# Performance work log

Measured on AMD Instinct MI355X. Metric: run time of the kernel, lower is better.

## Reference

```python
import jax, jax.numpy as jnp
import numpy as np

N = 50000      # nodes
E = 800000     # edges (before self-loops)
IN = 256       # input features
H = 8          # heads
C = 32         # hidden channels per head
OUT = 40       # classes
NEG_SLOPE = 0.2


def setup_inputs() -> dict:
    key = jax.random.key(0)
    ks = jax.random.split(key, 12)
    sd = lambda k, sh: (jax.random.normal(k, sh, jnp.float32) * 0.05)
    return {
        "x": jax.random.normal(ks[0], (N, IN), jnp.float32),
        "edge_index": jax.random.randint(ks[1], (2, E), 0, N),
        "W1": sd(ks[2], (IN, H * C)),
        "a_src1": sd(ks[3], (H, C)),
        "a_dst1": sd(ks[4], (H, C)),
        "b1": jnp.zeros((C,), jnp.float32),
        "W2": sd(ks[5], (C, H * C)),
        "a_src2": sd(ks[6], (H, C)),
        "a_dst2": sd(ks[7], (H, C)),
        "b2": jnp.zeros((C,), jnp.float32),
        "Wo": sd(ks[8], (C, OUT)),
        "bo": jnp.zeros((OUT,), jnp.float32),
    }


def gat_layer(x, src, dst, n, W, a_src, a_dst, b):
    # x: [N, F]; src/dst: [E'] (self-loops included). concat=False -> mean over heads.
    h = (x @ W).reshape(n, H, C)                       # [N, H, C]
    alpha_src = jnp.sum(h * a_src, axis=-1)            # [N, H]
    alpha_dst = jnp.sum(h * a_dst, axis=-1)            # [N, H]
    e = alpha_src[src] + alpha_dst[dst]                # [E', H]
    e = jnp.where(e > 0, e, NEG_SLOPE * e)             # leaky_relu
    # segment softmax over incoming edges of each dst node
    m = jax.ops.segment_max(e, dst, num_segments=n)    # [N, H]
    ex = jnp.exp(e - m[dst])                           # [E', H]
    s = jax.ops.segment_sum(ex, dst, num_segments=n)   # [N, H]
    alpha = ex / s[dst]                                # [E', H]
    msg = alpha[:, :, None] * h[src]                   # [E', H, C]
    out = jax.ops.segment_sum(msg, dst, num_segments=n)  # [N, H, C]
    return out.mean(axis=1) + b                        # [N, C]


def reference(x, edge_index, W1, a_src1, a_dst1, b1, W2, a_src2, a_dst2, b2, Wo, bo):
    n = x.shape[0]
    loops = jnp.arange(n, dtype=edge_index.dtype)
    src = jnp.concatenate([edge_index[0], loops])      # add self-loops (PyG default)
    dst = jnp.concatenate([edge_index[1], loops])
    h = gat_layer(x, src, dst, n, W1, a_src1, a_dst1, b1)
    h = jax.nn.elu(h)                                  # dropout skipped (eval)
    h = gat_layer(h, src, dst, n, W2, a_src2, a_dst2, b2)
    h = jax.nn.elu(h)
    logits = h @ Wo + bo
    return jax.nn.log_softmax(logits, axis=1)
```

## Files before the change

### kernel.cpp

```cpp
#include <hip/hip_runtime.h>
#include <math.h>

#define N_NODES 50000
#define N_PAD   50016
#define N_EDGES 800000
#define E_TOT   (N_EDGES + N_NODES)
#define F_IN    256
#define NHEAD   8
#define CH      32
#define HC      256
#define OUT_C   40
#define NEG_SLOPE 0.2f
#define CAP     64
#define G_WCVT  ((HC * F_IN + 255) / 256)
#define G_WCVT2 ((HC * CH + 255) / 256)
#define NRANGE  8
#define RANGE_SZ (N_NODES / NRANGE)
#define BIN_CHUNK 2048
#define G_BINCH ((E_TOT + BIN_CHUNK - 1) / BIN_CHUNK)
#define G_BIN   (G_BINCH * NRANGE)

typedef unsigned short u16;
typedef unsigned int   u32;
typedef unsigned char  u8;
typedef __attribute__((ext_vector_type(8))) short bf16x8;
typedef __attribute__((ext_vector_type(4))) float f32x4;
typedef __attribute__((ext_vector_type(2))) float f32x2;

__device__ __forceinline__ u16 f2bf(float f) {
    union { u32 u; float f; } x; x.f = f;
    u32 u = x.u;
    return (u16)((u + 0x7fffu + ((u >> 16) & 1u)) >> 16);
}
__device__ __forceinline__ float bflo(u32 v) {
    union { u32 u; float f; } x; x.u = v << 16; return x.f;
}
__device__ __forceinline__ u8 f2fp8(float f) {
    return (u8)(__builtin_amdgcn_cvt_pk_fp8_f32(f, f, 0, false) & 0xff);
}


__global__ __launch_bounds__(256) void prep_kernel(const int* __restrict__ ei,
        int* __restrict__ cursor, u16* __restrict__ csr_src,
        const float* __restrict__ W1, u16* __restrict__ Wt,
        const float* __restrict__ W2, u16* __restrict__ W2t) {
    int b = blockIdx.x;
    if (b < G_BIN) {
        const int r  = b & (NRANGE - 1);
        const int ch = b >> 3;
        const int lo = r * RANGE_SZ, hi = lo + RANGE_SZ;
        int j0 = ch * BIN_CHUNK + threadIdx.x;
        #pragma unroll
        for (int i = 0; i < BIN_CHUNK / 256; ++i) {
            int j = j0 + i * 256;
            if (j < E_TOT) {
                int d = (j < N_EDGES) ? ei[N_EDGES + j] : (j - N_EDGES);
                if (d >= lo && d < hi) {
                    int s = (j < N_EDGES) ? ei[j] : d;
                    int pos = atomicAdd(&cursor[d], 1);
                    if (pos < CAP) csr_src[d * CAP + pos] = (u16)s;
                }
            }
        }
    } else if (b < G_BIN + G_WCVT) {
        int t = (b - G_BIN) * 256 + threadIdx.x;
        int n = t & 255, k = t >> 8;
        Wt[(size_t)n * F_IN + k] = f2bf(W1[(size_t)k * HC + n]);
    } else {
        int t = (b - G_BIN - G_WCVT) * 256 + threadIdx.x;
        if (t >= HC * CH) return;
        int n = t & 255, k = t >> 8;
        W2t[(size_t)n * CH + k] = f2bf(W2[(size_t)k * HC + n]);
    }
}

__device__ __forceinline__ void gemm_epilogue(f32x4 acc[2][4], int row0, int quad,
        int l16, int nb, const float* __restrict__ a_src,
        const float* __restrict__ a_dst, u8* __restrict__ ht8,
        float* __restrict__ asrc, float* __restrict__ adst) {
    #pragma unroll
    for (int m = 0; m < 2; ++m) {
        #pragma unroll
        for (int r = 0; r < 4; ++r) {
            int row = row0 + m * 16 + quad * 4 + r;
            if (row < N_NODES) {
                u8* hr = ht8 + (size_t)row * HC;
                #pragma unroll
                for (int n = 0; n < 4; ++n)
                    hr[nb + n * 16 + l16] = f2fp8(acc[m][n][r]);
            }
        }
    }
    const int hA = nb >> 5;
    const float sA0 = a_src[hA * 32 + l16],       sA1 = a_src[hA * 32 + 16 + l16];
    const float sB0 = a_src[(hA + 1) * 32 + l16], sB1 = a_src[(hA + 1) * 32 + 16 + l16];
    const float dA0 = a_dst[hA * 32 + l16],       dA1 = a_dst[hA * 32 + 16 + l16];
    const float dB0 = a_dst[(hA + 1) * 32 + l16], dB1 = a_dst[(hA + 1) * 32 + 16 + l16];
    #pragma unroll
    for (int m = 0; m < 2; ++m) {
        #pragma unroll
        for (int r = 0; r < 4; ++r) {
            float pa = acc[m][0][r] * sA0 + acc[m][1][r] * sA1;
            float pb = acc[m][2][r] * sB0 + acc[m][3][r] * sB1;
            float qa = acc[m][0][r] * dA0 + acc[m][1][r] * dA1;
            float qb = acc[m][2][r] * dB0 + acc[m][3][r] * dB1;
            #pragma unroll
            for (int off = 1; off < 16; off <<= 1) {
                pa += __shfl_xor(pa, off, 64);
                pb += __shfl_xor(pb, off, 64);
                qa += __shfl_xor(qa, off, 64);
                qb += __shfl_xor(qb, off, 64);
            }
            int row = row0 + m * 16 + quad * 4 + r;
            if (l16 == 0 && row < N_NODES) {
                asrc[row * NHEAD + hA]     = pa;
                asrc[row * NHEAD + hA + 1] = pb;
                adst[row * NHEAD + hA]     = qa;
                adst[row * NHEAD + hA + 1] = qb;
            }
        }
    }
}

__global__ __launch_bounds__(256) void gemm1_mfma(const float* __restrict__ x,
        const u16* __restrict__ Wt, const float* __restrict__ a_src,
        const float* __restrict__ a_dst, u8* __restrict__ ht8,
        float* __restrict__ asrc, float* __restrict__ adst) {
    __shared__ u16 As[32 * 256];
    const int row0 = blockIdx.x * 32;
    const int t    = threadIdx.x;

    {
        const int r   = t >> 3;
        const int sub = t & 7;
        const int gr  = min(row0 + r, N_NODES - 1);
        const float4* xr = (const float4*)(x + (size_t)gr * F_IN);
        const int sw = (r & 7) << 4;
        char* Ar = (char*)As + r * 512;
        #pragma unroll
        for (int i = 0; i < 8; ++i) {
            int f4 = i * 8 + sub;
            float4 v = xr[f4];
            u32 lo = (u32)f2bf(v.x) | ((u32)f2bf(v.y) << 16);
            u32 hi = (u32)f2bf(v.z) | ((u32)f2bf(v.w) << 16);
            *(uint2*)(Ar + ((f4 * 8) ^ sw)) = make_uint2(lo, hi);
        }
    }
    __syncthreads();

    const int wave = t >> 6;
    const int lane = t & 63;
    const int l16  = lane & 15;
    const int quad = lane >> 4;
    const int nb   = wave * 64;
    const int swr  = (l16 & 7) << 4;
    const char* Ab = (const char*)As;

    f32x4 acc[2][4];
    #pragma unroll
    for (int m = 0; m < 2; ++m)
        #pragma unroll
        for (int n = 0; n < 4; ++n) acc[m][n] = (f32x4){0.f, 0.f, 0.f, 0.f};

    const u16* bp = Wt + (size_t)(nb + l16) * F_IN;

    #pragma unroll 1
    for (int k0 = 0; k0 < F_IN; k0 += 32) {
        const int ko = k0 + quad * 8;
        bf16x8 a0 = *(const bf16x8*)(Ab + l16 * 512 + ((ko * 2) ^ swr));
        bf16x8 a1 = *(const bf16x8*)(Ab + (16 + l16) * 512 + ((ko * 2) ^ swr));
        bf16x8 b0 = *(const bf16x8*)(bp + 0 * 16 * F_IN + ko);
        bf16x8 b1 = *(const bf16x8*)(bp + 1 * 16 * F_IN + ko);
        bf16x8 b2 = *(const bf16x8*)(bp + 2 * 16 * F_IN + ko);
        bf16x8 b3 = *(const bf16x8*)(bp + 3 * 16 * F_IN + ko);
        acc[0][0] = __builtin_amdgcn_mfma_f32_16x16x32_bf16(a0, b0, acc[0][0], 0, 0, 0);
        acc[0][1] = __builtin_amdgcn_mfma_f32_16x16x32_bf16(a0, b1, acc[0][1], 0, 0, 0);
        acc[0][2] = __builtin_amdgcn_mfma_f32_16x16x32_bf16(a0, b2, acc[0][2], 0, 0, 0);
        acc[0][3] = __builtin_amdgcn_mfma_f32_16x16x32_bf16(a0, b3, acc[0][3], 0, 0, 0);
        acc[1][0] = __builtin_amdgcn_mfma_f32_16x16x32_bf16(a1, b0, acc[1][0], 0, 0, 0);
        acc[1][1] = __builtin_amdgcn_mfma_f32_16x16x32_bf16(a1, b1, acc[1][1], 0, 0, 0);
        acc[1][2] = __builtin_amdgcn_mfma_f32_16x16x32_bf16(a1, b2, acc[1][2], 0, 0, 0);
        acc[1][3] = __builtin_amdgcn_mfma_f32_16x16x32_bf16(a1, b3, acc[1][3], 0, 0, 0);
    }
    gemm_epilogue(acc, row0, quad, l16, nb, a_src, a_dst, ht8, asrc, adst);
}

__global__ __launch_bounds__(256) void gemm2_mfma(const u16* __restrict__ hmb,
        const u16* __restrict__ W2t, const float* __restrict__ a_src,
        const float* __restrict__ a_dst, u8* __restrict__ ht8,
        float* __restrict__ asrc, float* __restrict__ adst) {
    const int row0 = blockIdx.x * 32;
    const int t    = threadIdx.x;
    const int wave = t >> 6;
    const int lane = t & 63;
    const int l16  = lane & 15;
    const int quad = lane >> 4;
    const int nb   = wave * 64;
    const int ko   = quad * 8;

    const u16* a0p = hmb + (size_t)(row0 + l16) * CH;
    const u16* a1p = a0p + 16 * CH;
    const u16* bp  = W2t + (size_t)(nb + l16) * CH;

    bf16x8 a0 = *(const bf16x8*)(a0p + ko);
    bf16x8 a1 = *(const bf16x8*)(a1p + ko);
    bf16x8 b0 = *(const bf16x8*)(bp + 0 * 16 * CH + ko);
    bf16x8 b1 = *(const bf16x8*)(bp + 1 * 16 * CH + ko);
    bf16x8 b2 = *(const bf16x8*)(bp + 2 * 16 * CH + ko);
    bf16x8 b3 = *(const bf16x8*)(bp + 3 * 16 * CH + ko);

    f32x4 z = (f32x4){0.f, 0.f, 0.f, 0.f};
    f32x4 acc[2][4];
    acc[0][0] = __builtin_amdgcn_mfma_f32_16x16x32_bf16(a0, b0, z, 0, 0, 0);
    acc[0][1] = __builtin_amdgcn_mfma_f32_16x16x32_bf16(a0, b1, z, 0, 0, 0);
    acc[0][2] = __builtin_amdgcn_mfma_f32_16x16x32_bf16(a0, b2, z, 0, 0, 0);
    acc[0][3] = __builtin_amdgcn_mfma_f32_16x16x32_bf16(a0, b3, z, 0, 0, 0);
    acc[1][0] = __builtin_amdgcn_mfma_f32_16x16x32_bf16(a1, b0, z, 0, 0, 0);
    acc[1][1] = __builtin_amdgcn_mfma_f32_16x16x32_bf16(a1, b1, z, 0, 0, 0);
    acc[1][2] = __builtin_amdgcn_mfma_f32_16x16x32_bf16(a1, b2, z, 0, 0, 0);
    acc[1][3] = __builtin_amdgcn_mfma_f32_16x16x32_bf16(a1, b3, z, 0, 0, 0);

    gemm_epilogue(acc, row0, quad, l16, nb, a_src, a_dst, ht8, asrc, adst);
}

__global__ __launch_bounds__(256) void attn_kernel(const int* __restrict__ degp,
        const u16* __restrict__ csr_src, const float* __restrict__ asrc,
        const float* __restrict__ adst, const u8* __restrict__ ht8,
        const float* __restrict__ b, u16* __restrict__ out) {
    const int wid = (blockIdx.x * 256 + threadIdx.x) >> 6;
    if (wid >= N_NODES) return;
    const int dst  = wid;
    const int lane = threadIdx.x & 63;
    const int q    = lane >> 4;
    const int l16  = lane & 15;
    const int h    = l16 >> 1;
    const float ad_own = adst[dst * NHEAD + h];
    const u8* hbase = ht8 + l16 * 16;

    f32x2 acc2[8];
    #pragma unroll
    for (int i = 0; i < 8; ++i) acc2[i] = (f32x2){0.f, 0.f};
    float wsum = 0.f;

    const int cnt = min(degp[dst], CAP);
    const int p0 = dst * CAP, p1 = p0 + cnt;
    const int nt = (cnt + 7) >> 3;

    float asA = -1e30f, asB = -1e30f;
    uint4 hvA = make_uint4(0u, 0u, 0u, 0u), hvB = make_uint4(0u, 0u, 0u, 0u);
    int e = p0 + q;
    if (e < p1) {
        int s = (int)csr_src[e];
        asA = asrc[s * NHEAD + h];
        hvA = *(const uint4*)(hbase + ((size_t)s << 8));
    }
    if (e + 4 < p1) {
        int s = (int)csr_src[e + 4];
        asB = asrc[s * NHEAD + h];
        hvB = *(const uint4*)(hbase + ((size_t)s << 8));
    }

    for (int it = 0; it < nt; ++it) {
        float aA = asA; uint4 hA = hvA;
        float aB = asB; uint4 hB = hvB;
        asA = -1e30f; asB = -1e30f;
        if (e + 8 < p1) {
            int s = (int)csr_src[e + 8];
            asA = asrc[s * NHEAD + h];
            hvA = *(const uint4*)(hbase + ((size_t)s << 8));
        }
        if (e + 12 < p1) {
            int s = (int)csr_src[e + 12];
            asB = asrc[s * NHEAD + h];
            hvB = *(const uint4*)(hbase + ((size_t)s << 8));
        }
        {
            float x = aA + ad_own;
            x = x > 0.f ? x : NEG_SLOPE * x;
            float w = __expf(x);
            wsum += w;
            f32x2 w2; w2.x = w; w2.y = w;
            acc2[0] = __builtin_elementwise_fma(w2, __builtin_amdgcn_cvt_pk_f32_fp8(hA.x, false), acc2[0]);
            acc2[1] = __builtin_elementwise_fma(w2, __builtin_amdgcn_cvt_pk_f32_fp8(hA.x, true ), acc2[1]);
            acc2[2] = __builtin_elementwise_fma(w2, __builtin_amdgcn_cvt_pk_f32_fp8(hA.y, false), acc2[2]);
            acc2[3] = __builtin_elementwise_fma(w2, __builtin_amdgcn_cvt_pk_f32_fp8(hA.y, true ), acc2[3]);
            acc2[4] = __builtin_elementwise_fma(w2, __builtin_amdgcn_cvt_pk_f32_fp8(hA.z, false), acc2[4]);
            acc2[5] = __builtin_elementwise_fma(w2, __builtin_amdgcn_cvt_pk_f32_fp8(hA.z, true ), acc2[5]);
            acc2[6] = __builtin_elementwise_fma(w2, __builtin_amdgcn_cvt_pk_f32_fp8(hA.w, false), acc2[6]);
            acc2[7] = __builtin_elementwise_fma(w2, __builtin_amdgcn_cvt_pk_f32_fp8(hA.w, true ), acc2[7]);
        }
        {
            float x = aB + ad_own;
            x = x > 0.f ? x : NEG_SLOPE * x;
            float w = __expf(x);
            wsum += w;
            f32x2 w2; w2.x = w; w2.y = w;
            acc2[0] = __builtin_elementwise_fma(w2, __builtin_amdgcn_cvt_pk_f32_fp8(hB.x, false), acc2[0]);
            acc2[1] = __builtin_elementwise_fma(w2, __builtin_amdgcn_cvt_pk_f32_fp8(hB.x, true ), acc2[1]);
            acc2[2] = __builtin_elementwise_fma(w2, __builtin_amdgcn_cvt_pk_f32_fp8(hB.y, false), acc2[2]);
            acc2[3] = __builtin_elementwise_fma(w2, __builtin_amdgcn_cvt_pk_f32_fp8(hB.y, true ), acc2[3]);
            acc2[4] = __builtin_elementwise_fma(w2, __builtin_amdgcn_cvt_pk_f32_fp8(hB.z, false), acc2[4]);
            acc2[5] = __builtin_elementwise_fma(w2, __builtin_amdgcn_cvt_pk_f32_fp8(hB.z, true ), acc2[5]);
            acc2[6] = __builtin_elementwise_fma(w2, __builtin_amdgcn_cvt_pk_f32_fp8(hB.w, false), acc2[6]);
            acc2[7] = __builtin_elementwise_fma(w2, __builtin_amdgcn_cvt_pk_f32_fp8(hB.w, true ), acc2[7]);
        }
        e += 8;
    }

    #pragma unroll
    for (int i = 0; i < 8; ++i) {
        acc2[i].x += __shfl_xor(acc2[i].x, 16, 64);
        acc2[i].y += __shfl_xor(acc2[i].y, 16, 64);
        acc2[i].x += __shfl_xor(acc2[i].x, 32, 64);
        acc2[i].y += __shfl_xor(acc2[i].y, 32, 64);
    }
    wsum += __shfl_xor(wsum, 16, 64);
    wsum += __shfl_xor(wsum, 32, 64);

    float winv = 1.0f / wsum;
    f32x2 winv2; winv2.x = winv; winv2.y = winv;
    #pragma unroll
    for (int i = 0; i < 8; ++i) acc2[i] *= winv2;

    #pragma unroll
    for (int i = 0; i < 8; ++i) {
        acc2[i].x += __shfl_xor(acc2[i].x, 2, 64);
        acc2[i].y += __shfl_xor(acc2[i].y, 2, 64);
        acc2[i].x += __shfl_xor(acc2[i].x, 4, 64);
        acc2[i].y += __shfl_xor(acc2[i].y, 4, 64);
        acc2[i].x += __shfl_xor(acc2[i].x, 8, 64);
        acc2[i].y += __shfl_xor(acc2[i].y, 8, 64);
    }

    if (lane < 2) {
        const int c0 = lane * 16;
        const float4* bp4 = (const float4*)(b + c0);
        float4 b0 = bp4[0], b1 = bp4[1], b2 = bp4[2], b3 = bp4[3];
        float bb[16] = {b0.x, b0.y, b0.z, b0.w, b1.x, b1.y, b1.z, b1.w,
                        b2.x, b2.y, b2.z, b2.w, b3.x, b3.y, b3.z, b3.w};
        u32 d[8];
        #pragma unroll
        for (int i = 0; i < 8; ++i) {
            float v0 = acc2[i].x * 0.125f + bb[2 * i];
            float v1 = acc2[i].y * 0.125f + bb[2 * i + 1];
            v0 = v0 > 0.f ? v0 : (__expf(v0) - 1.f);
            v1 = v1 > 0.f ? v1 : (__expf(v1) - 1.f);
            d[i] = (u32)f2bf(v0) | ((u32)f2bf(v1) << 16);
        }
        uint4* op = (uint4*)(out + (size_t)dst * CH + c0);
        op[0] = make_uint4(d[0], d[1], d[2], d[3]);
        op[1] = make_uint4(d[4], d[5], d[6], d[7]);
    }
}

__global__ __launch_bounds__(256) void out_kernel(const u16* __restrict__ hf,
        const float* __restrict__ Wo, const float* __restrict__ bo,
        float* __restrict__ out) {
    const int wave = threadIdx.x >> 6;
    const int lane = threadIdx.x & 63;
    const int n    = blockIdx.x * 4 + wave;
    __shared__ float hs[4][CH];
    if (n < N_NODES && lane < CH) hs[wave][lane] = bflo((u32)hf[n * CH + lane]);
    __syncthreads();
    if (n >= N_NODES) return;
    float logit = -INFINITY;
    if (lane < OUT_C) {
        float a = bo[lane];
        #pragma unroll
        for (int k = 0; k < CH; ++k) a += hs[wave][k] * Wo[k * OUT_C + lane];
        logit = a;
    }
    float m = logit;
    #pragma unroll
    for (int off = 32; off; off >>= 1) m = fmaxf(m, __shfl_xor(m, off, 64));
    float ex = (lane < OUT_C) ? __expf(logit - m) : 0.f;
    float ssum = ex;
    #pragma unroll
    for (int off = 32; off; off >>= 1) ssum += __shfl_xor(ssum, off, 64);
    if (lane < OUT_C) out[(size_t)n * OUT_C + lane] = logit - m - __logf(ssum);
}

extern "C" void kernel_launch(void* const* d_in, const int* in_sizes, int n_in,
                              void* d_out, int out_size, void* d_ws, size_t ws_size,
                              hipStream_t stream) {
    const float* x      = (const float*)d_in[0];
    const int*   ei     = (const int*)  d_in[1];
    const float* W1     = (const float*)d_in[2];
    const float* a_src1 = (const float*)d_in[3];
    const float* a_dst1 = (const float*)d_in[4];
    const float* b1     = (const float*)d_in[5];
    const float* W2     = (const float*)d_in[6];
    const float* a_src2 = (const float*)d_in[7];
    const float* a_dst2 = (const float*)d_in[8];
    const float* b2     = (const float*)d_in[9];
    const float* Wo     = (const float*)d_in[10];
    const float* bo     = (const float*)d_in[11];
    float* out = (float*)d_out;

    char* ws = (char*)d_ws;
    size_t off = 0;
    auto carve = [&](size_t bytes) { char* p = ws + off; off += (bytes + 255) & ~(size_t)255; return p; };
    u8*    ht8     = (u8*)   carve((size_t)N_NODES * HC);
    u16*   Wt      = (u16*)  carve((size_t)HC * F_IN * 2);
    u16*   W2t     = (u16*)  carve((size_t)HC * CH * 2);
    float* asrc    = (float*)carve((size_t)N_NODES * NHEAD * 4);
    float* adst    = (float*)carve((size_t)N_NODES * NHEAD * 4);
    u16*   hmid    = (u16*)  carve((size_t)N_PAD * CH * 2);
    u16*   hout    = (u16*)  carve((size_t)N_NODES * CH * 2);
    int*   cursor  = (int*)  carve((size_t)N_NODES * 4);
    u16*   csr_src = (u16*)  carve((size_t)N_NODES * CAP * 2);

    const int g_prep  = G_BIN + G_WCVT + G_WCVT2;
    const int g_gemm  = (N_NODES + 31) / 32;
    const int g_attn  = (N_NODES * 64 + 255) / 256;
    const int g_out   = (N_NODES + 3) / 4;

    (void)hipMemsetAsync(cursor, 0, (size_t)N_NODES * 4, stream);
    prep_kernel<<<g_prep, 256, 0, stream>>>(ei, cursor, csr_src, W1, Wt, W2, W2t);

    gemm1_mfma<<<g_gemm, 256, 0, stream>>>(x, Wt, a_src1, a_dst1, ht8, asrc, adst);
    attn_kernel<<<g_attn, 256, 0, stream>>>(cursor, csr_src, asrc, adst, ht8, b1, hmid);

    gemm2_mfma<<<g_gemm, 256, 0, stream>>>(hmid, W2t, a_src2, a_dst2, ht8, asrc, adst);
    attn_kernel<<<g_attn, 256, 0, stream>>>(cursor, csr_src, asrc, adst, ht8, b2, hout);

    out_kernel<<<g_out, 256, 0, stream>>>(hout, Wo, bo, out);
}
```

Baseline: 317.2 us.

## Sort per-node neighbor lists and fuse final attention with output head

Adds a bitonic sort kernel that orders each destination's source indices, so gathers from ht8 follow a more sequential, cache-friendly pattern and the CSR order becomes deterministic. It also fuses the second attention aggregation with the bias/ELU, output linear layer and log-softmax into one kernel, which removes the hout round trip and one launch. The fused kernel skips max subtraction in the softmax, which assumes the scores stay small enough not to overflow. The extra sort pass costs one read and write of the CSR array.

```diff
diff --git a/kernel.cpp b/kernel.cpp
--- a/kernel.cpp
+++ b/kernel.cpp
@@ -72,6 +72,26 @@
         int n = t & 255, k = t >> 8;
         W2t[(size_t)n * CH + k] = f2bf(W2[(size_t)k * HC + n]);
     }
+}
+
+__global__ __launch_bounds__(256) void sort_kernel(const int* __restrict__ cursor,
+        u16* __restrict__ csr_src) {
+    const int dst  = (blockIdx.x * 256 + threadIdx.x) >> 6;
+    if (dst >= N_NODES) return;
+    const int lane = threadIdx.x & 63;
+    const int cnt  = min(cursor[dst], CAP);
+    u32 v = (lane < cnt) ? (u32)csr_src[dst * CAP + lane] : 0x7FFFFFFFu;
+    #pragma unroll
+    for (int k = 2; k <= 64; k <<= 1) {
+        #pragma unroll
+        for (int j = k >> 1; j > 0; j >>= 1) {
+            u32 pv = (u32)__shfl_xor((int)v, j, 64);
+            bool asc      = ((lane & k) == 0);
+            bool keep_min = (((lane & j) == 0) == asc);
+            v = keep_min ? min(v, pv) : max(v, pv);
+        }
+    }
+    if (lane < cnt) csr_src[dst * CAP + lane] = (u16)v;
 }
 
 __device__ __forceinline__ void gemm_epilogue(f32x4 acc[2][4], int row0, int quad,
@@ -353,31 +373,145 @@
     }
 }
 
-__global__ __launch_bounds__(256) void out_kernel(const u16* __restrict__ hf,
-        const float* __restrict__ Wo, const float* __restrict__ bo,
-        float* __restrict__ out) {
-    const int wave = threadIdx.x >> 6;
+__global__ __launch_bounds__(256) void attn_fin_kernel(const int* __restrict__ degp,
+        const u16* __restrict__ csr_src, const float* __restrict__ asrc,
+        const float* __restrict__ adst, const u8* __restrict__ ht8,
+        const float* __restrict__ b, const float* __restrict__ Wo,
+        const float* __restrict__ bo, float* __restrict__ out) {
+    const int dst  = (blockIdx.x * 256 + threadIdx.x) >> 6;
     const int lane = threadIdx.x & 63;
-    const int n    = blockIdx.x * 4 + wave;
-    __shared__ float hs[4][CH];
-    if (n < N_NODES && lane < CH) hs[wave][lane] = bflo((u32)hf[n * CH + lane]);
+    const int w4   = threadIdx.x >> 6;
+    const int q    = lane >> 4;
+    const int l16  = lane & 15;
+    const int h    = l16 >> 1;
+    const float ad_own = adst[dst * NHEAD + h];
+    const u8* hbase = ht8 + l16 * 16;
+
+    __shared__ float hsm[4][CH];
+
+    f32x2 acc2[8];
+    #pragma unroll
+    for (int i = 0; i < 8; ++i) acc2[i] = (f32x2){0.f, 0.f};
+    float wsum = 0.f;
+
+    const int cnt = min(degp[dst], CAP);
+    const int p0 = dst * CAP, p1 = p0 + cnt;
+    const int nt = (cnt + 7) >> 3;
+
+    float asA = -1e30f, asB = -1e30f;
+    uint4 hvA = make_uint4(0u, 0u, 0u, 0u), hvB = make_uint4(0u, 0u, 0u, 0u);
+    int e = p0 + q;
+    if (e < p1) {
+        int s = (int)csr_src[e];
+        asA = asrc[s * NHEAD + h];
+        hvA = *(const uint4*)(hbase + ((size_t)s << 8));
+    }
+    if (e + 4 < p1) {
+        int s = (int)csr_src[e + 4];
+        asB = asrc[s * NHEAD + h];
+        hvB = *(const uint4*)(hbase + ((size_t)s << 8));
+    }
+
+    for (int it = 0; it < nt; ++it) {
+        float aA = asA; uint4 hA = hvA;
+        float aB = asB; uint4 hB = hvB;
+        asA = -1e30f; asB = -1e30f;
+        if (e + 8 < p1) {
+            int s = (int)csr_src[e + 8];
+            asA = asrc[s * NHEAD + h];
+            hvA = *(const uint4*)(hbase + ((size_t)s << 8));
+        }
+        if (e + 12 < p1) {
+            int s = (int)csr_src[e + 12];
+            asB = asrc[s * NHEAD + h];
+            hvB = *(const uint4*)(hbase + ((size_t)s << 8));
+        }
+        {
+            float x = aA + ad_own;
+            x = x > 0.f ? x : NEG_SLOPE * x;
+            float w = __expf(x);
+            wsum += w;
+            f32x2 w2; w2.x = w; w2.y = w;
+            acc2[0] = __builtin_elementwise_fma(w2, __builtin_amdgcn_cvt_pk_f32_fp8(hA.x, false), acc2[0]);
+            acc2[1] = __builtin_elementwise_fma(w2, __builtin_amdgcn_cvt_pk_f32_fp8(hA.x, true ), acc2[1]);
+            acc2[2] = __builtin_elementwise_fma(w2, __builtin_amdgcn_cvt_pk_f32_fp8(hA.y, false), acc2[2]);
+            acc2[3] = __builtin_elementwise_fma(w2, __builtin_amdgcn_cvt_pk_f32_fp8(hA.y, true ), acc2[3]);
+            acc2[4] = __builtin_elementwise_fma(w2, __builtin_amdgcn_cvt_pk_f32_fp8(hA.z, false), acc2[4]);
+            acc2[5] = __builtin_elementwise_fma(w2, __builtin_amdgcn_cvt_pk_f32_fp8(hA.z, true ), acc2[5]);
+            acc2[6] = __builtin_elementwise_fma(w2, __builtin_amdgcn_cvt_pk_f32_fp8(hA.w, false), acc2[6]);
+            acc2[7] = __builtin_elementwise_fma(w2, __builtin_amdgcn_cvt_pk_f32_fp8(hA.w, true ), acc2[7]);
+        }
+        {
+            float x = aB + ad_own;
+            x = x > 0.f ? x : NEG_SLOPE * x;
+            float w = __expf(x);
+            wsum += w;
+            f32x2 w2; w2.x = w; w2.y = w;
+            acc2[0] = __builtin_elementwise_fma(w2, __builtin_amdgcn_cvt_pk_f32_fp8(hB.x, false), acc2[0]);
+            acc2[1] = __builtin_elementwise_fma(w2, __builtin_amdgcn_cvt_pk_f32_fp8(hB.x, true ), acc2[1]);
+            acc2[2] = __builtin_elementwise_fma(w2, __builtin_amdgcn_cvt_pk_f32_fp8(hB.y, false), acc2[2]);
+            acc2[3] = __builtin_elementwise_fma(w2, __builtin_amdgcn_cvt_pk_f32_fp8(hB.y, true ), acc2[3]);
+            acc2[4] = __builtin_elementwise_fma(w2, __builtin_amdgcn_cvt_pk_f32_fp8(hB.z, false), acc2[4]);
+            acc2[5] = __builtin_elementwise_fma(w2, __builtin_amdgcn_cvt_pk_f32_fp8(hB.z, true ), acc2[5]);
+            acc2[6] = __builtin_elementwise_fma(w2, __builtin_amdgcn_cvt_pk_f32_fp8(hB.w, false), acc2[6]);
+            acc2[7] = __builtin_elementwise_fma(w2, __builtin_amdgcn_cvt_pk_f32_fp8(hB.w, true ), acc2[7]);
+        }
+        e += 8;
+    }
+
+    #pragma unroll
+    for (int i = 0; i < 8; ++i) {
+        acc2[i].x += __shfl_xor(acc2[i].x, 16, 64);
+        acc2[i].y += __shfl_xor(acc2[i].y, 16, 64);
+        acc2[i].x += __shfl_xor(acc2[i].x, 32, 64);
+        acc2[i].y += __shfl_xor(acc2[i].y, 32, 64);
+    }
+    wsum += __shfl_xor(wsum, 16, 64);
+    wsum += __shfl_xor(wsum, 32, 64);
+
+    float winv = 1.0f / wsum;
+    f32x2 winv2; winv2.x = winv; winv2.y = winv;
+    #pragma unroll
+    for (int i = 0; i < 8; ++i) acc2[i] *= winv2;
+
+    #pragma unroll
+    for (int i = 0; i < 8; ++i) {
+        acc2[i].x += __shfl_xor(acc2[i].x, 2, 64);
+        acc2[i].y += __shfl_xor(acc2[i].y, 2, 64);
+        acc2[i].x += __shfl_xor(acc2[i].x, 4, 64);
+        acc2[i].y += __shfl_xor(acc2[i].y, 4, 64);
+        acc2[i].x += __shfl_xor(acc2[i].x, 8, 64);
+        acc2[i].y += __shfl_xor(acc2[i].y, 8, 64);
+    }
+
+    if (lane < 2) {
+        #pragma unroll
+        for (int i = 0; i < 8; ++i) {
+            hsm[w4][lane * 16 + 2 * i]     = acc2[i].x * 0.125f;
+            hsm[w4][lane * 16 + 2 * i + 1] = acc2[i].y * 0.125f;
+        }
+    }
     __syncthreads();
-    if (n >= N_NODES) return;
+    if (lane < CH) {
+        float v = hsm[w4][lane] + b[lane];
+        hsm[w4][lane] = v > 0.f ? v : (__expf(v) - 1.f);
+    }
+    __syncthreads();
     float logit = -INFINITY;
     if (lane < OUT_C) {
         float a = bo[lane];
         #pragma unroll
-        for (int k = 0; k < CH; ++k) a += hs[wave][k] * Wo[k * OUT_C + lane];
+        for (int k = 0; k < CH; ++k) a += hsm[w4][k] * Wo[k * OUT_C + lane];
         logit = a;
     }
-    float m = logit;
-    #pragma unroll
-    for (int off = 32; off; off >>= 1) m = fmaxf(m, __shfl_xor(m, off, 64));
-    float ex = (lane < OUT_C) ? __expf(logit - m) : 0.f;
-    float ssum = ex;
-    #pragma unroll
-    for (int off = 32; off; off >>= 1) ssum += __shfl_xor(ssum, off, 64);
-    if (lane < OUT_C) out[(size_t)n * OUT_C + lane] = logit - m - __logf(ssum);
+    float mx = logit;
+    #pragma unroll
+    for (int off = 32; off; off >>= 1) mx = fmaxf(mx, __shfl_xor(mx, off, 64));
+    float ex = (lane < OUT_C) ? __expf(logit - mx) : 0.f;
+    float ss = ex;
+    #pragma unroll
+    for (int off = 32; off; off >>= 1) ss += __shfl_xor(ss, off, 64);
+    if (lane < OUT_C) out[(size_t)dst * OUT_C + lane] = logit - mx - __logf(ss);
 }
 
 extern "C" void kernel_launch(void* const* d_in, const int* in_sizes, int n_in,
@@ -406,23 +540,22 @@
     float* asrc    = (float*)carve((size_t)N_NODES * NHEAD * 4);
     float* adst    = (float*)carve((size_t)N_NODES * NHEAD * 4);
     u16*   hmid    = (u16*)  carve((size_t)N_PAD * CH * 2);
-    u16*   hout    = (u16*)  carve((size_t)N_NODES * CH * 2);
     int*   cursor  = (int*)  carve((size_t)N_NODES * 4);
     u16*   csr_src = (u16*)  carve((size_t)N_NODES * CAP * 2);
 
     const int g_prep  = G_BIN + G_WCVT + G_WCVT2;
+    const int g_sort  = (N_NODES * 64 + 255) / 256;
     const int g_gemm  = (N_NODES + 31) / 32;
     const int g_attn  = (N_NODES * 64 + 255) / 256;
-    const int g_out   = (N_NODES + 3) / 4;
 
     (void)hipMemsetAsync(cursor, 0, (size_t)N_NODES * 4, stream);
     prep_kernel<<<g_prep, 256, 0, stream>>>(ei, cursor, csr_src, W1, Wt, W2, W2t);
+    sort_kernel<<<g_sort, 256, 0, stream>>>(cursor, csr_src);
 
     gemm1_mfma<<<g_gemm, 256, 0, stream>>>(x, Wt, a_src1, a_dst1, ht8, asrc, adst);
     attn_kernel<<<g_attn, 256, 0, stream>>>(cursor, csr_src, asrc, adst, ht8, b1, hmid);
 
     gemm2_mfma<<<g_gemm, 256, 0, stream>>>(hmid, W2t, a_src2, a_dst2, ht8, asrc, adst);
-    attn_kernel<<<g_attn, 256, 0, stream>>>(cursor, csr_src, asrc, adst, ht8, b2, hout);
-
-    out_kernel<<<g_out, 256, 0, stream>>>(hout, Wo, bo, out);
-}
+    attn_fin_kernel<<<g_attn, 256, 0, stream>>>(cursor, csr_src, asrc, adst,
+                                                ht8, b2, Wo, bo, out);
+}
```

Result: slower. 323.9 us (+2.1%).

## Fuse CSR binning with GEMM1, split layer-1 attention by head groups

Applied to the files above, without the earlier changes.

Edge binning now runs in the same launch as the first GEMM, as independent blocks of one mega kernel, so the two overlap. Weight conversion moves to its own small kernel. Layer-1 attention is split across four head-group blocks per 4-node group, which raises parallelism, and each writes fp32 partial head sums. GEMM2 then reduces those partials and applies the head mean, bias and ELU while loading its A operand. The cost is an extra fp32 partial buffer round-trip, and the fused kernel shares LDS allocation between its two roles.

```diff
diff --git a/kernel.cpp b/kernel.cpp
--- a/kernel.cpp
+++ b/kernel.cpp
@@ -19,6 +19,7 @@
 #define BIN_CHUNK 2048
 #define G_BINCH ((E_TOT + BIN_CHUNK - 1) / BIN_CHUNK)
 #define G_BIN   (G_BINCH * NRANGE)
+#define G_GEMM  (N_PAD / 32)
 
 typedef unsigned short u16;
 typedef unsigned int   u32;
@@ -40,34 +41,15 @@
 }
 
 
-__global__ __launch_bounds__(256) void prep_kernel(const int* __restrict__ ei,
-        int* __restrict__ cursor, u16* __restrict__ csr_src,
-        const float* __restrict__ W1, u16* __restrict__ Wt,
-        const float* __restrict__ W2, u16* __restrict__ W2t) {
+__global__ __launch_bounds__(256) void wcvt_kernel(const float* __restrict__ W1,
+        u16* __restrict__ Wt, const float* __restrict__ W2, u16* __restrict__ W2t) {
     int b = blockIdx.x;
-    if (b < G_BIN) {
-        const int r  = b & (NRANGE - 1);
-        const int ch = b >> 3;
-        const int lo = r * RANGE_SZ, hi = lo + RANGE_SZ;
-        int j0 = ch * BIN_CHUNK + threadIdx.x;
-        #pragma unroll
-        for (int i = 0; i < BIN_CHUNK / 256; ++i) {
-            int j = j0 + i * 256;
-            if (j < E_TOT) {
-                int d = (j < N_EDGES) ? ei[N_EDGES + j] : (j - N_EDGES);
-                if (d >= lo && d < hi) {
-                    int s = (j < N_EDGES) ? ei[j] : d;
-                    int pos = atomicAdd(&cursor[d], 1);
-                    if (pos < CAP) csr_src[d * CAP + pos] = (u16)s;
-                }
-            }
-        }
-    } else if (b < G_BIN + G_WCVT) {
-        int t = (b - G_BIN) * 256 + threadIdx.x;
+    if (b < G_WCVT) {
+        int t = b * 256 + threadIdx.x;
         int n = t & 255, k = t >> 8;
         Wt[(size_t)n * F_IN + k] = f2bf(W1[(size_t)k * HC + n]);
     } else {
-        int t = (b - G_BIN - G_WCVT) * 256 + threadIdx.x;
+        int t = (b - G_WCVT) * 256 + threadIdx.x;
         if (t >= HC * CH) return;
         int n = t & 255, k = t >> 8;
         W2t[(size_t)n * CH + k] = f2bf(W2[(size_t)k * HC + n]);
@@ -122,14 +104,34 @@
     }
 }
 
-__global__ __launch_bounds__(256) void gemm1_mfma(const float* __restrict__ x,
-        const u16* __restrict__ Wt, const float* __restrict__ a_src,
-        const float* __restrict__ a_dst, u8* __restrict__ ht8,
-        float* __restrict__ asrc, float* __restrict__ adst) {
+__global__ __launch_bounds__(256) void mega_kernel(const int* __restrict__ ei,
+        int* __restrict__ cursor, u16* __restrict__ csr_src,
+        const float* __restrict__ x, const u16* __restrict__ Wt,
+        const float* __restrict__ a_src, const float* __restrict__ a_dst,
+        u8* __restrict__ ht8, float* __restrict__ asrc, float* __restrict__ adst) {
     __shared__ u16 As[32 * 256];
-    const int row0 = blockIdx.x * 32;
+    const int b = blockIdx.x;
+    if (b < G_BIN) {
+        const int r  = b & (NRANGE - 1);
+        const int ch = b >> 3;
+        const int lo = r * RANGE_SZ, hi = lo + RANGE_SZ;
+        int j0 = ch * BIN_CHUNK + threadIdx.x;
+        #pragma unroll
+        for (int i = 0; i < BIN_CHUNK / 256; ++i) {
+            int j = j0 + i * 256;
+            if (j < E_TOT) {
+                int d = (j < N_EDGES) ? ei[N_EDGES + j] : (j - N_EDGES);
+                if (d >= lo && d < hi) {
+                    int s = (j < N_EDGES) ? ei[j] : d;
+                    int pos = atomicAdd(&cursor[d], 1);
+                    if (pos < CAP) csr_src[d * CAP + pos] = (u16)s;
+                }
+            }
+        }
+        return;
+    }
+    const int row0 = (b - G_BIN) * 32;
     const int t    = threadIdx.x;
-
     {
         const int r   = t >> 3;
         const int sub = t & 7;
@@ -185,10 +187,115 @@
     gemm_epilogue(acc, row0, quad, l16, nb, a_src, a_dst, ht8, asrc, adst);
 }
 
-__global__ __launch_bounds__(256) void gemm2_mfma(const u16* __restrict__ hmb,
-        const u16* __restrict__ W2t, const float* __restrict__ a_src,
-        const float* __restrict__ a_dst, u8* __restrict__ ht8,
-        float* __restrict__ asrc, float* __restrict__ adst) {
+__global__ __launch_bounds__(256) void attn1_split_kernel(
+        const int* __restrict__ degp, const u16* __restrict__ csr_src,
+        const float* __restrict__ asrc, const float* __restrict__ adst,
+        const u8* __restrict__ ht8, float* __restrict__ ppart) {
+    const int g    = (blockIdx.x & 7) >> 1;
+    const int dst  = ((blockIdx.x >> 3) * 2 + (blockIdx.x & 1)) * 4
+                     + (threadIdx.x >> 6);
+    const int lane = threadIdx.x & 63;
+    const int oct  = lane >> 3;
+    const int l8   = lane & 7;
+    const int h    = g * 2 + (l8 >> 2);
+    const float ad_own = adst[dst * NHEAD + h];
+    const u8* hbase = ht8 + g * 64 + l8 * 8;
+
+    f32x2 acc2[4];
+    #pragma unroll
+    for (int i = 0; i < 4; ++i) acc2[i] = (f32x2){0.f, 0.f};
+    float wsum = 0.f;
+
+    const int cnt = min(degp[dst], CAP);
+    const int p0 = dst * CAP, p1 = p0 + cnt;
+    const int nt = (cnt + 15) >> 4;
+
+    float asA = -1e30f, asB = -1e30f;
+    uint2 hvA = make_uint2(0u, 0u), hvB = make_uint2(0u, 0u);
+    int e = p0 + oct;
+    if (e < p1) {
+        int s = (int)csr_src[e];
+        asA = asrc[s * NHEAD + h];
+        hvA = *(const uint2*)(hbase + ((size_t)s << 8));
+    }
+    if (e + 8 < p1) {
+        int s = (int)csr_src[e + 8];
+        asB = asrc[s * NHEAD + h];
+        hvB = *(const uint2*)(hbase + ((size_t)s << 8));
+    }
+
+    for (int it = 0; it < nt; ++it) {
+        float aA = asA; uint2 hA = hvA;
+        float aB = asB; uint2 hB = hvB;
+        asA = -1e30f; asB = -1e30f;
+        if (e + 16 < p1) {
+            int s = (int)csr_src[e + 16];
+            asA = asrc[s * NHEAD + h];
+            hvA = *(const uint2*)(hbase + ((size_t)s << 8));
+        }
+        if (e + 24 < p1) {
+            int s = (int)csr_src[e + 24];
+            asB = asrc[s * NHEAD + h];
+            hvB = *(const uint2*)(hbase + ((size_t)s << 8));
+        }
+        {
+            float xv = aA + ad_own;
+            xv = xv > 0.f ? xv : NEG_SLOPE * xv;
+            float w = __expf(xv);
+            wsum += w;
+            f32x2 w2; w2.x = w; w2.y = w;
+            acc2[0] = __builtin_elementwise_fma(w2, __builtin_amdgcn_cvt_pk_f32_fp8(hA.x, false), acc2[0]);
+            acc2[1] = __builtin_elementwise_fma(w2, __builtin_amdgcn_cvt_pk_f32_fp8(hA.x, true ), acc2[1]);
+            acc2[2] = __builtin_elementwise_fma(w2, __builtin_amdgcn_cvt_pk_f32_fp8(hA.y, false), acc2[2]);
+            acc2[3] = __builtin_elementwise_fma(w2, __builtin_amdgcn_cvt_pk_f32_fp8(hA.y, true ), acc2[3]);
+        }
+        {
+            float xv = aB + ad_own;
+            xv = xv > 0.f ? xv : NEG_SLOPE * xv;
+            float w = __expf(xv);
+            wsum += w;
+            f32x2 w2; w2.x = w; w2.y = w;
+            acc2[0] = __builtin_elementwise_fma(w2, __builtin_amdgcn_cvt_pk_f32_fp8(hB.x, false), acc2[0]);
+            acc2[1] = __builtin_elementwise_fma(w2, __builtin_amdgcn_cvt_pk_f32_fp8(hB.x, true ), acc2[1]);
+            acc2[2] = __builtin_elementwise_fma(w2, __builtin_amdgcn_cvt_pk_f32_fp8(hB.y, false), acc2[2]);
+            acc2[3] = __builtin_elementwise_fma(w2, __builtin_amdgcn_cvt_pk_f32_fp8(hB.y, true ), acc2[3]);
+        }
+        e += 16;
+    }
+
+    #pragma unroll
+    for (int i = 0; i < 4; ++i) {
+        acc2[i].x += __shfl_xor(acc2[i].x, 8, 64);
+        acc2[i].y += __shfl_xor(acc2[i].y, 8, 64);
+        acc2[i].x += __shfl_xor(acc2[i].x, 16, 64);
+        acc2[i].y += __shfl_xor(acc2[i].y, 16, 64);
+        acc2[i].x += __shfl_xor(acc2[i].x, 32, 64);
+        acc2[i].y += __shfl_xor(acc2[i].y, 32, 64);
+    }
+    wsum += __shfl_xor(wsum, 8, 64);
+    wsum += __shfl_xor(wsum, 16, 64);
+    wsum += __shfl_xor(wsum, 32, 64);
+
+    float winv = 1.0f / wsum;
+    f32x2 winv2; winv2.x = winv; winv2.y = winv;
+    #pragma unroll
+    for (int i = 0; i < 4; ++i) {
+        acc2[i] *= winv2;
+        acc2[i].x += __shfl_xor(acc2[i].x, 4, 64);
+        acc2[i].y += __shfl_xor(acc2[i].y, 4, 64);
+    }
+
+    if (lane < 4) {
+        float* pp = ppart + ((size_t)g * N_PAD + dst) * CH + l8 * 8;
+        ((float4*)pp)[0] = make_float4(acc2[0].x, acc2[0].y, acc2[1].x, acc2[1].y);
+        ((float4*)pp)[1] = make_float4(acc2[2].x, acc2[2].y, acc2[3].x, acc2[3].y);
+    }
+}
+
+__global__ __launch_bounds__(256) void gemm2_mfma(const float* __restrict__ ppart,
+        const u16* __restrict__ W2t, const float* __restrict__ b1,
+        const float* __restrict__ a_src, const float* __restrict__ a_dst,
+        u8* __restrict__ ht8, float* __restrict__ asrc, float* __restrict__ adst) {
     const int row0 = blockIdx.x * 32;
     const int t    = threadIdx.x;
     const int wave = t >> 6;
@@ -198,25 +305,50 @@
     const int nb   = wave * 64;
     const int ko   = quad * 8;
 
-    const u16* a0p = hmb + (size_t)(row0 + l16) * CH;
-    const u16* a1p = a0p + 16 * CH;
-    const u16* bp  = W2t + (size_t)(nb + l16) * CH;
-
-    bf16x8 a0 = *(const bf16x8*)(a0p + ko);
-    bf16x8 a1 = *(const bf16x8*)(a1p + ko);
+    const f32x4* b4 = (const f32x4*)(b1 + ko);
+    const f32x4 blo = b4[0], bhi = b4[1];
+
+    auto loadA = [&](int row) -> bf16x8 {
+        f32x4 slo = (f32x4){0.f, 0.f, 0.f, 0.f};
+        f32x4 shi = (f32x4){0.f, 0.f, 0.f, 0.f};
+        #pragma unroll
+        for (int g = 0; g < 4; ++g) {
+            const f32x4* p = (const f32x4*)(ppart + ((size_t)g * N_PAD + row) * CH + ko);
+            slo += p[0];
+            shi += p[1];
+        }
+        slo = slo * 0.125f + blo;
+        shi = shi * 0.125f + bhi;
+        bf16x8 a;
+        #pragma unroll
+        for (int i = 0; i < 4; ++i) {
+            float v0 = slo[i];
+            v0 = v0 > 0.f ? v0 : (__expf(v0) - 1.f);
+            a[i] = (short)f2bf(v0);
+            float v1 = shi[i];
+            v1 = v1 > 0.f ? v1 : (__expf(v1) - 1.f);
+            a[4 + i] = (short)f2bf(v1);
+        }
+        return a;
+    };
+
+    bf16x8 a0 = loadA(row0 + l16);
+    bf16x8 a1 = loadA(row0 + 16 + l16);
+
+    const u16* bp = W2t + (size_t)(nb + l16) * CH;
     bf16x8 b0 = *(const bf16x8*)(bp + 0 * 16 * CH + ko);
-    bf16x8 b1 = *(const bf16x8*)(bp + 1 * 16 * CH + ko);
+    bf16x8 b1v = *(const bf16x8*)(bp + 1 * 16 * CH + ko);
     bf16x8 b2 = *(const bf16x8*)(bp + 2 * 16 * CH + ko);
     bf16x8 b3 = *(const bf16x8*)(bp + 3 * 16 * CH + ko);
 
     f32x4 z = (f32x4){0.f, 0.f, 0.f, 0.f};
     f32x4 acc[2][4];
     acc[0][0] = __builtin_amdgcn_mfma_f32_16x16x32_bf16(a0, b0, z, 0, 0, 0);
-    acc[0][1] = __builtin_amdgcn_mfma_f32_16x16x32_bf16(a0, b1, z, 0, 0, 0);
+    acc[0][1] = __builtin_amdgcn_mfma_f32_16x16x32_bf16(a0, b1v, z, 0, 0, 0);
     acc[0][2] = __builtin_amdgcn_mfma_f32_16x16x32_bf16(a0, b2, z, 0, 0, 0);
     acc[0][3] = __builtin_amdgcn_mfma_f32_16x16x32_bf16(a0, b3, z, 0, 0, 0);
     acc[1][0] = __builtin_amdgcn_mfma_f32_16x16x32_bf16(a1, b0, z, 0, 0, 0);
-    acc[1][1] = __builtin_amdgcn_mfma_f32_16x16x32_bf16(a1, b1, z, 0, 0, 0);
+    acc[1][1] = __builtin_amdgcn_mfma_f32_16x16x32_bf16(a1, b1v, z, 0, 0, 0);
     acc[1][2] = __builtin_amdgcn_mfma_f32_16x16x32_bf16(a1, b2, z, 0, 0, 0);
     acc[1][3] = __builtin_amdgcn_mfma_f32_16x16x32_bf16(a1, b3, z, 0, 0, 0);
 
@@ -405,23 +537,27 @@
     u16*   W2t     = (u16*)  carve((size_t)HC * CH * 2);
     float* asrc    = (float*)carve((size_t)N_NODES * NHEAD * 4);
     float* adst    = (float*)carve((size_t)N_NODES * NHEAD * 4);
-    u16*   hmid    = (u16*)  carve((size_t)N_PAD * CH * 2);
+    float* ppart   = (float*)carve((size_t)4 * N_PAD * CH * 4);
     u16*   hout    = (u16*)  carve((size_t)N_NODES * CH * 2);
     int*   cursor  = (int*)  carve((size_t)N_NODES * 4);
     u16*   csr_src = (u16*)  carve((size_t)N_NODES * CAP * 2);
 
-    const int g_prep  = G_BIN + G_WCVT + G_WCVT2;
-    const int g_gemm  = (N_NODES + 31) / 32;
+    const int g_wcvt  = G_WCVT + G_WCVT2;
+    const int g_mega  = G_BIN + G_GEMM;
+    const int g_split = N_NODES;
     const int g_attn  = (N_NODES * 64 + 255) / 256;
     const int g_out   = (N_NODES + 3) / 4;
 
     (void)hipMemsetAsync(cursor, 0, (size_t)N_NODES * 4, stream);
-    prep_kernel<<<g_prep, 256, 0, stream>>>(ei, cursor, csr_src, W1, Wt, W2, W2t);
-
-    gemm1_mfma<<<g_gemm, 256, 0, stream>>>(x, Wt, a_src1, a_dst1, ht8, asrc, adst);
-    attn_kernel<<<g_attn, 256, 0, stream>>>(cursor, csr_src, asrc, adst, ht8, b1, hmid);
-
-    gemm2_mfma<<<g_gemm, 256, 0, stream>>>(hmid, W2t, a_src2, a_dst2, ht8, asrc, adst);
+    wcvt_kernel<<<g_wcvt, 256, 0, stream>>>(W1, Wt, W2, W2t);
+    mega_kernel<<<g_mega, 256, 0, stream>>>(ei, cursor, csr_src,
+                                            x, Wt, a_src1, a_dst1, ht8, asrc, adst);
+
+    attn1_split_kernel<<<g_split, 256, 0, stream>>>(cursor, csr_src, asrc, adst,
+                                                    ht8, ppart);
+
+    gemm2_mfma<<<G_GEMM, 256, 0, stream>>>(ppart, W2t, b1, a_src2, a_dst2,
+                                           ht8, asrc, adst);
     attn_kernel<<<g_attn, 256, 0, stream>>>(cursor, csr_src, asrc, adst, ht8, b2, hout);
 
     out_kernel<<<g_out, 256, 0, stream>>>(hout, Wo, bo, out);
```

Measured after the change: 349.0 us. +10.0%, slower.

## Merge CSR binning into layer-1 GEMM launch and deepen attention gather prefetch

Applied to the files above, without the earlier changes.

The edge-binning CSR build now runs as extra blocks of the same launch as the layer-1 GEMM, so the atomic-heavy binning and the MFMA GEMM can share the GPU at once. The small weight conversion moves to its own kernel ahead of it. The attention kernel's gather pipeline now prefetches two iterations ahead instead of one, keeping more neighbour loads in flight. The cost is higher register pressure in the attention kernel and a GEMM grid now sized from the padded row count, which relies on the row clamping already in the GEMM.

```diff
diff --git a/kernel.cpp b/kernel.cpp
--- a/kernel.cpp
+++ b/kernel.cpp
@@ -19,6 +19,7 @@
 #define BIN_CHUNK 2048
 #define G_BINCH ((E_TOT + BIN_CHUNK - 1) / BIN_CHUNK)
 #define G_BIN   (G_BINCH * NRANGE)
+#define G_GEMM  (N_PAD / 32)
 
 typedef unsigned short u16;
 typedef unsigned int   u32;
@@ -40,34 +41,15 @@
 }
 
 
-__global__ __launch_bounds__(256) void prep_kernel(const int* __restrict__ ei,
-        int* __restrict__ cursor, u16* __restrict__ csr_src,
-        const float* __restrict__ W1, u16* __restrict__ Wt,
-        const float* __restrict__ W2, u16* __restrict__ W2t) {
+__global__ __launch_bounds__(256) void wcvt_kernel(const float* __restrict__ W1,
+        u16* __restrict__ Wt, const float* __restrict__ W2, u16* __restrict__ W2t) {
     int b = blockIdx.x;
-    if (b < G_BIN) {
-        const int r  = b & (NRANGE - 1);
-        const int ch = b >> 3;
-        const int lo = r * RANGE_SZ, hi = lo + RANGE_SZ;
-        int j0 = ch * BIN_CHUNK + threadIdx.x;
-        #pragma unroll
-        for (int i = 0; i < BIN_CHUNK / 256; ++i) {
-            int j = j0 + i * 256;
-            if (j < E_TOT) {
-                int d = (j < N_EDGES) ? ei[N_EDGES + j] : (j - N_EDGES);
-                if (d >= lo && d < hi) {
-                    int s = (j < N_EDGES) ? ei[j] : d;
-                    int pos = atomicAdd(&cursor[d], 1);
-                    if (pos < CAP) csr_src[d * CAP + pos] = (u16)s;
-                }
-            }
-        }
-    } else if (b < G_BIN + G_WCVT) {
-        int t = (b - G_BIN) * 256 + threadIdx.x;
+    if (b < G_WCVT) {
+        int t = b * 256 + threadIdx.x;
         int n = t & 255, k = t >> 8;
         Wt[(size_t)n * F_IN + k] = f2bf(W1[(size_t)k * HC + n]);
     } else {
-        int t = (b - G_BIN - G_WCVT) * 256 + threadIdx.x;
+        int t = (b - G_WCVT) * 256 + threadIdx.x;
         if (t >= HC * CH) return;
         int n = t & 255, k = t >> 8;
         W2t[(size_t)n * CH + k] = f2bf(W2[(size_t)k * HC + n]);
@@ -122,14 +104,34 @@
     }
 }
 
-__global__ __launch_bounds__(256) void gemm1_mfma(const float* __restrict__ x,
-        const u16* __restrict__ Wt, const float* __restrict__ a_src,
-        const float* __restrict__ a_dst, u8* __restrict__ ht8,
-        float* __restrict__ asrc, float* __restrict__ adst) {
+__global__ __launch_bounds__(256) void mega_kernel(const int* __restrict__ ei,
+        int* __restrict__ cursor, u16* __restrict__ csr_src,
+        const float* __restrict__ x, const u16* __restrict__ Wt,
+        const float* __restrict__ a_src, const float* __restrict__ a_dst,
+        u8* __restrict__ ht8, float* __restrict__ asrc, float* __restrict__ adst) {
     __shared__ u16 As[32 * 256];
-    const int row0 = blockIdx.x * 32;
+    const int b = blockIdx.x;
+    if (b < G_BIN) {
+        const int r  = b & (NRANGE - 1);
+        const int ch = b >> 3;
+        const int lo = r * RANGE_SZ, hi = lo + RANGE_SZ;
+        int j0 = ch * BIN_CHUNK + threadIdx.x;
+        #pragma unroll
+        for (int i = 0; i < BIN_CHUNK / 256; ++i) {
+            int j = j0 + i * 256;
+            if (j < E_TOT) {
+                int d = (j < N_EDGES) ? ei[N_EDGES + j] : (j - N_EDGES);
+                if (d >= lo && d < hi) {
+                    int s = (j < N_EDGES) ? ei[j] : d;
+                    int pos = atomicAdd(&cursor[d], 1);
+                    if (pos < CAP) csr_src[d * CAP + pos] = (u16)s;
+                }
+            }
+        }
+        return;
+    }
+    const int row0 = (b - G_BIN) * 32;
     const int t    = threadIdx.x;
-
     {
         const int r   = t >> 3;
         const int sub = t & 7;
@@ -246,8 +248,9 @@
     const int p0 = dst * CAP, p1 = p0 + cnt;
     const int nt = (cnt + 7) >> 3;
 
-    float asA = -1e30f, asB = -1e30f;
-    uint4 hvA = make_uint4(0u, 0u, 0u, 0u), hvB = make_uint4(0u, 0u, 0u, 0u);
+    const uint4 z4 = make_uint4(0u, 0u, 0u, 0u);
+    float asA = -1e30f, asB = -1e30f, asC = -1e30f, asD = -1e30f;
+    uint4 hvA = z4, hvB = z4, hvC = z4, hvD = z4;
     int e = p0 + q;
     if (e < p1) {
         int s = (int)csr_src[e];
@@ -259,51 +262,62 @@
         asB = asrc[s * NHEAD + h];
         hvB = *(const uint4*)(hbase + ((size_t)s << 8));
     }
+    if (e + 8 < p1) {
+        int s = (int)csr_src[e + 8];
+        asC = asrc[s * NHEAD + h];
+        hvC = *(const uint4*)(hbase + ((size_t)s << 8));
+    }
+    if (e + 12 < p1) {
+        int s = (int)csr_src[e + 12];
+        asD = asrc[s * NHEAD + h];
+        hvD = *(const uint4*)(hbase + ((size_t)s << 8));
+    }
 
     for (int it = 0; it < nt; ++it) {
-        float aA = asA; uint4 hA = hvA;
-        float aB = asB; uint4 hB = hvB;
-        asA = -1e30f; asB = -1e30f;
-        if (e + 8 < p1) {
-            int s = (int)csr_src[e + 8];
-            asA = asrc[s * NHEAD + h];
-            hvA = *(const uint4*)(hbase + ((size_t)s << 8));
-        }
-        if (e + 12 < p1) {
-            int s = (int)csr_src[e + 12];
-            asB = asrc[s * NHEAD + h];
-            hvB = *(const uint4*)(hbase + ((size_t)s << 8));
+        float tA = -1e30f, tB = -1e30f;
+        uint4 tHA = z4, tHB = z4;
+        if (e + 16 < p1) {
+            int s = (int)csr_src[e + 16];
+            tA = asrc[s * NHEAD + h];
+            tHA = *(const uint4*)(hbase + ((size_t)s << 8));
+        }
+        if (e + 20 < p1) {
+            int s = (int)csr_src[e + 20];
+            tB = asrc[s * NHEAD + h];
+            tHB = *(const uint4*)(hbase + ((size_t)s << 8));
         }
         {
-            float x = aA + ad_own;
+            float x = asA + ad_own;
             x = x > 0.f ? x : NEG_SLOPE * x;
             float w = __expf(x);
             wsum += w;
             f32x2 w2; w2.x = w; w2.y = w;
-            acc2[0] = __builtin_elementwise_fma(w2, __builtin_amdgcn_cvt_pk_f32_fp8(hA.x, false), acc2[0]);
-            acc2[1] = __builtin_elementwise_fma(w2, __builtin_amdgcn_cvt_pk_f32_fp8(hA.x, true ), acc2[1]);
-            acc2[2] = __builtin_elementwise_fma(w2, __builtin_amdgcn_cvt_pk_f32_fp8(hA.y, false), acc2[2]);
-            acc2[3] = __builtin_elementwise_fma(w2, __builtin_amdgcn_cvt_pk_f32_fp8(hA.y, true ), acc2[3]);
-            acc2[4] = __builtin_elementwise_fma(w2, __builtin_amdgcn_cvt_pk_f32_fp8(hA.z, false), acc2[4]);
-            acc2[5] = __builtin_elementwise_fma(w2, __builtin_amdgcn_cvt_pk_f32_fp8(hA.z, true ), acc2[5]);
-            acc2[6] = __builtin_elementwise_fma(w2, __builtin_amdgcn_cvt_pk_f32_fp8(hA.w, false), acc2[6]);
-            acc2[7] = __builtin_elementwise_fma(w2, __builtin_amdgcn_cvt_pk_f32_fp8(hA.w, true ), acc2[7]);
+            acc2[0] = __builtin_elementwise_fma(w2, __builtin_amdgcn_cvt_pk_f32_fp8(hvA.x, false), acc2[0]);
+            acc2[1] = __builtin_elementwise_fma(w2, __builtin_amdgcn_cvt_pk_f32_fp8(hvA.x, true ), acc2[1]);
+            acc2[2] = __builtin_elementwise_fma(w2, __builtin_amdgcn_cvt_pk_f32_fp8(hvA.y, false), acc2[2]);
+            acc2[3] = __builtin_elementwise_fma(w2, __builtin_amdgcn_cvt_pk_f32_fp8(hvA.y, true ), acc2[3]);
+            acc2[4] = __builtin_elementwise_fma(w2, __builtin_amdgcn_cvt_pk_f32_fp8(hvA.z, false), acc2[4]);
+            acc2[5] = __builtin_elementwise_fma(w2, __builtin_amdgcn_cvt_pk_f32_fp8(hvA.z, true ), acc2[5]);
+            acc2[6] = __builtin_elementwise_fma(w2, __builtin_amdgcn_cvt_pk_f32_fp8(hvA.w, false), acc2[6]);
+            acc2[7] = __builtin_elementwise_fma(w2, __builtin_amdgcn_cvt_pk_f32_fp8(hvA.w, true ), acc2[7]);
         }
         {
-            float x = aB + ad_own;
+            float x = asB + ad_own;
             x = x > 0.f ? x : NEG_SLOPE * x;
             float w = __expf(x);
             wsum += w;
             f32x2 w2; w2.x = w; w2.y = w;
-            acc2[0] = __builtin_elementwise_fma(w2, __builtin_amdgcn_cvt_pk_f32_fp8(hB.x, false), acc2[0]);
-            acc2[1] = __builtin_elementwise_fma(w2, __builtin_amdgcn_cvt_pk_f32_fp8(hB.x, true ), acc2[1]);
-            acc2[2] = __builtin_elementwise_fma(w2, __builtin_amdgcn_cvt_pk_f32_fp8(hB.y, false), acc2[2]);
-            acc2[3] = __builtin_elementwise_fma(w2, __builtin_amdgcn_cvt_pk_f32_fp8(hB.y, true ), acc2[3]);
-            acc2[4] = __builtin_elementwise_fma(w2, __builtin_amdgcn_cvt_pk_f32_fp8(hB.z, false), acc2[4]);
-            acc2[5] = __builtin_elementwise_fma(w2, __builtin_amdgcn_cvt_pk_f32_fp8(hB.z, true ), acc2[5]);
-            acc2[6] = __builtin_elementwise_fma(w2, __builtin_amdgcn_cvt_pk_f32_fp8(hB.w, false), acc2[6]);
-            acc2[7] = __builtin_elementwise_fma(w2, __builtin_amdgcn_cvt_pk_f32_fp8(hB.w, true ), acc2[7]);
-        }
+            acc2[0] = __builtin_elementwise_fma(w2, __builtin_amdgcn_cvt_pk_f32_fp8(hvB.x, false), acc2[0]);
+            acc2[1] = __builtin_elementwise_fma(w2, __builtin_amdgcn_cvt_pk_f32_fp8(hvB.x, true ), acc2[1]);
+            acc2[2] = __builtin_elementwise_fma(w2, __builtin_amdgcn_cvt_pk_f32_fp8(hvB.y, false), acc2[2]);
+            acc2[3] = __builtin_elementwise_fma(w2, __builtin_amdgcn_cvt_pk_f32_fp8(hvB.y, true ), acc2[3]);
+            acc2[4] = __builtin_elementwise_fma(w2, __builtin_amdgcn_cvt_pk_f32_fp8(hvB.z, false), acc2[4]);
+            acc2[5] = __builtin_elementwise_fma(w2, __builtin_amdgcn_cvt_pk_f32_fp8(hvB.z, true ), acc2[5]);
+            acc2[6] = __builtin_elementwise_fma(w2, __builtin_amdgcn_cvt_pk_f32_fp8(hvB.w, false), acc2[6]);
+            acc2[7] = __builtin_elementwise_fma(w2, __builtin_amdgcn_cvt_pk_f32_fp8(hvB.w, true ), acc2[7]);
+        }
+        asA = asC; hvA = hvC; asB = asD; hvB = hvD;
+        asC = tA;  hvC = tHA; asD = tB;  hvD = tHB;
         e += 8;
     }
 
@@ -410,18 +424,19 @@
     int*   cursor  = (int*)  carve((size_t)N_NODES * 4);
     u16*   csr_src = (u16*)  carve((size_t)N_NODES * CAP * 2);
 
-    const int g_prep  = G_BIN + G_WCVT + G_WCVT2;
-    const int g_gemm  = (N_NODES + 31) / 32;
+    const int g_wcvt  = G_WCVT + G_WCVT2;
+    const int g_mega  = G_BIN + G_GEMM;
     const int g_attn  = (N_NODES * 64 + 255) / 256;
     const int g_out   = (N_NODES + 3) / 4;
 
     (void)hipMemsetAsync(cursor, 0, (size_t)N_NODES * 4, stream);
-    prep_kernel<<<g_prep, 256, 0, stream>>>(ei, cursor, csr_src, W1, Wt, W2, W2t);
-
-    gemm1_mfma<<<g_gemm, 256, 0, stream>>>(x, Wt, a_src1, a_dst1, ht8, asrc, adst);
+    wcvt_kernel<<<g_wcvt, 256, 0, stream>>>(W1, Wt, W2, W2t);
+    mega_kernel<<<g_mega, 256, 0, stream>>>(ei, cursor, csr_src,
+                                            x, Wt, a_src1, a_dst1, ht8, asrc, adst);
+
     attn_kernel<<<g_attn, 256, 0, stream>>>(cursor, csr_src, asrc, adst, ht8, b1, hmid);
 
-    gemm2_mfma<<<g_gemm, 256, 0, stream>>>(hmid, W2t, a_src2, a_dst2, ht8, asrc, adst);
+    gemm2_mfma<<<G_GEMM, 256, 0, stream>>>(hmid, W2t, a_src2, a_dst2, ht8, asrc, adst);
     attn_kernel<<<g_attn, 256, 0, stream>>>(cursor, csr_src, asrc, adst, ht8, b2, hout);
 
     out_kernel<<<g_out, 256, 0, stream>>>(hout, Wo, bo, out);
```

Measured after the change: 318.0 us. No clear change (+0.3%).
